# Kernel optimization log

Measured on AMD Instinct MI355X. Metric: run time of the kernel, lower is better.

## Reference

```python
import jax, jax.numpy as jnp
import numpy as np

NEG = -1.0e30  # stand-in for -inf, safe under logaddexp in fp32
DEN_SCALE = 1.0


def _ctc_forward(logp, targets, in_lens, tgt_lens):
    """Log-semiring forward (tot score) over the numerator lattice:
    CTC topology composed with the linear target FSA. logp: [B,T,C] (blank=0),
    targets: [B,U] in [1, C-1]. Returns [B] numerator log-scores."""
    B, T, C = logp.shape
    U = targets.shape[1]
    S = 2 * U + 1  # extended label sequence: blank-interleaved
    ext = jnp.zeros((B, S), dtype=jnp.int32).at[:, 1::2].set(targets.astype(jnp.int32))
    # skip transition s-2 -> s allowed only for non-blank, non-repeated labels
    skip_ok = jnp.concatenate(
        [jnp.zeros((B, 2), dtype=bool), (ext[:, 2:] != 0) & (ext[:, 2:] != ext[:, :-2])],
        axis=1,
    )
    emit0 = jnp.take_along_axis(logp[:, 0], ext, axis=1)  # [B,S]
    alpha = jnp.full((B, S), NEG, dtype=logp.dtype)
    alpha = alpha.at[:, 0].set(emit0[:, 0]).at[:, 1].set(emit0[:, 1])
    logp_t = jnp.swapaxes(logp, 0, 1)  # [T,B,C]

    def step(alpha, xs):
        t, lp = xs
        a1 = jnp.concatenate([jnp.full((B, 1), NEG, alpha.dtype), alpha[:, :-1]], axis=1)
        a2 = jnp.concatenate([jnp.full((B, 2), NEG, alpha.dtype), alpha[:, :-2]], axis=1)
        cand = jnp.logaddexp(jnp.logaddexp(alpha, a1), jnp.where(skip_ok, a2, NEG))
        new = cand + jnp.take_along_axis(lp, ext, axis=1)
        alpha = jnp.where((t < in_lens)[:, None], new, alpha)  # freeze past utterance end
        return alpha, None

    alpha, _ = jax.lax.scan(step, alpha, (jnp.arange(1, T), logp_t[1:]))
    last = (2 * tgt_lens).astype(jnp.int32)  # final states: last blank / last label
    a_last = jnp.take_along_axis(alpha, last[:, None], axis=1)[:, 0]
    a_prev = jnp.take_along_axis(alpha, (last - 1)[:, None], axis=1)[:, 0]
    return jnp.logaddexp(a_last, a_prev)


def _den_forward(logp, trans, start, in_lens):
    """Log-semiring forward over the dense denominator graph (bigram token LM):
    states = token classes, transition log-weights trans[C,C]. Returns [B]."""
    B, T, C = logp.shape
    alpha = start[None, :] + logp[:, 0]  # [B,C]
    logp_t = jnp.swapaxes(logp, 0, 1)  # [T,B,C]

    def step(alpha, xs):
        t, lp = xs
        new = jax.nn.logsumexp(alpha[:, :, None] + trans[None], axis=1) + lp
        alpha = jnp.where((t < in_lens)[:, None], new, alpha)
        return alpha, None

    alpha, _ = jax.lax.scan(step, alpha, (jnp.arange(1, T), logp_t[1:]))
    return jax.nn.logsumexp(alpha, axis=1)


def setup_inputs() -> dict:
    key = jax.random.key(0)
    ks = jax.random.split(key, 6)
    B, T, C, U = 32, 2000, 256, 200
    log_probs = jax.nn.log_softmax(jax.random.normal(ks[0], (B, T, C), dtype=jnp.float32), axis=-1)
    targets = jax.random.randint(ks[1], (B, U), 1, C)
    input_lengths = jax.random.randint(ks[2], (B,), T // 2, T + 1)
    target_lengths = jax.random.randint(ks[3], (B,), U // 2, U + 1)
    den_transitions = jax.random.normal(ks[4], (C, C), dtype=jnp.float32) * 0.1
    den_start = jax.random.normal(ks[5], (C,), dtype=jnp.float32) * 0.1
    return {
        "log_probs": log_probs,
        "targets": targets,
        "input_lengths": input_lengths,
        "target_lengths": target_lengths,
        "den_transitions": den_transitions,
        "den_start": den_start,
    }


def reference(log_probs, targets, input_lengths, target_lengths, den_transitions, den_start):
    logp = jax.nn.log_softmax(log_probs, axis=-1)  # idempotent if already normalized
    B, T, C = logp.shape
    U = targets.shape[1]
    in_lens = jnp.clip(input_lengths, 2 * U + 1, T).astype(jnp.int32)
    tgt_lens = jnp.clip(target_lengths, 1, U).astype(jnp.int32)
    tgt = jnp.clip(targets, 1, C - 1)  # blank=0 excluded from targets
    num = _ctc_forward(logp, tgt, in_lens, tgt_lens)
    den = _den_forward(logp, den_transitions, den_start, in_lens)
    tot = num - DEN_SCALE * den  # LF-MMI per-utterance objective
    valid = tot > 0.5 * NEG  # mimic get_tot_objf_and_num_frames -inf filtering
    n = jnp.maximum(jnp.sum(valid), 1)
    return -jnp.sum(jnp.where(valid, tot, 0.0)) / n
```

## Files before the change

kernel.cpp:

```cpp
#include <hip/hip_runtime.h>
#include <stdint.h>
#include <stddef.h>

#define NEGF (-1.0e30f)

typedef __attribute__((ext_vector_type(2))) _Float16 half2_t;
typedef uint32_t u32x16 __attribute__((ext_vector_type(16)));

constexpr int Bn = 32;
constexpr int Tn = 2000;
constexpr int Cn = 256;
constexpr int Un = 200;
constexpr int Sn = 2 * Un + 1;
constexpr float Kn = 4096.0f;

__device__ __forceinline__ float fdot2f(uint32_t a, uint32_t b, float c) {
  half2_t ha = __builtin_bit_cast(half2_t, a);
  half2_t hb = __builtin_bit_cast(half2_t, b);
#if __has_builtin(__builtin_amdgcn_fdot2)
  return __builtin_amdgcn_fdot2(ha, hb, c, false);
#else
  return c + (float)ha.x * (float)hb.x + (float)ha.y * (float)hb.y;
#endif
}

template <int CTRL>
__device__ __forceinline__ float dppf(float x) {
#if __has_builtin(__builtin_amdgcn_update_dpp)
  int xi = __builtin_bit_cast(int, x);
  int y = __builtin_amdgcn_update_dpp(0, xi, CTRL, 0xF, 0xF, false);
  return __builtin_bit_cast(float, y);
#else
  return x;
#endif
}
#define dpp_x1(v) dppf<0xB1>(v)
#define dpp_x2(v) dppf<0x4E>(v)
#define dpp_x7(v) dppf<0x141>(v)

__device__ __forceinline__ uint32_t packe(float a, float b) {
  half2_t h;
  h.x = (_Float16)a;
  h.y = (_Float16)b;
  return __builtin_bit_cast(uint32_t, h);
}

__device__ __forceinline__ float lse3(float a, float b, float c) {
  float m = fmaxf(fmaxf(a, b), c);
  return m + __logf(__expf(a - m) + __expf(b - m) + __expf(c - m));
}

__device__ __forceinline__ int clampi(int v, int lo, int hi) {
  return v < lo ? lo : (v > hi ? hi : v);
}

__device__ __forceinline__ void barrier_nodrain() {
  asm volatile("s_waitcnt lgkmcnt(0)" ::: "memory");
  __builtin_amdgcn_s_barrier();
  asm volatile("" ::: "memory");
}

__global__ __launch_bounds__(256)
__attribute__((amdgpu_waves_per_eu(1, 1)))
void fwd_kernel(
    const float* __restrict__ logp, const int* __restrict__ targets,
    const int* __restrict__ in_lens, const int* __restrict__ tgt_lens,
    const float* __restrict__ trans, const float* __restrict__ start,
    float* __restrict__ ws) {
  const int tid = threadIdx.x;
  const int bid = blockIdx.x;

  if (bid < Bn) {
    const int b = bid;
    const int L = clampi(in_lens[b], Sn, Tn);
    const int q = tid & 7;
    const int u = tid >> 3;
    const int jw = u + 32 * q;

    __shared__ __align__(16) char eaLDS[2 * 8 * 80];
    __shared__ float sred[4];

    const float* trow = trans;
#define EP(c, m) packe(__expf(trow[(32 * q + 2 * (m)) * Cn + (c)]), \
                       __expf(trow[(32 * q + 2 * (m) + 1) * Cn + (c)]))
#define MKCOL(c)                                                          \
  (u32x16){EP(c, 0),  EP(c, 1),  EP(c, 2),  EP(c, 3),  EP(c, 4),          \
           EP(c, 5),  EP(c, 6),  EP(c, 7),  EP(c, 8),  EP(c, 9),          \
           EP(c, 10), EP(c, 11), EP(c, 12), EP(c, 13), EP(c, 14), EP(c, 15)}
    u32x16 E0 = MKCOL(u + 0);
    u32x16 E1 = MKCOL(u + 32);
    u32x16 E2 = MKCOL(u + 64);
    u32x16 E3 = MKCOL(u + 96);
    u32x16 E4 = MKCOL(u + 128);
    u32x16 E5 = MKCOL(u + 160);
    u32x16 E6 = MKCOL(u + 192);
    u32x16 E7 = MKCOL(u + 224);
#undef MKCOL
#undef EP

    const float* lpb = logp + (size_t)b * Tn * Cn;
    const char* rbase0 = eaLDS + 80 * q;
    char* wptr0 = eaLDS + 80 * q + 2 * u;

    float G = -__logf(Kn);
    *(_Float16*)(wptr0) = (_Float16)(Kn * __expf(start[jw] + lpb[jw]));
    float lp0 = lpb[Cn + jw];
    float lp1 = lpb[(size_t)2 * Cn + jw];
    __syncthreads();

    const uint32_t ONE2 = 0x3C003C00u;
    const bool q4 = (q & 4) != 0, q2 = (q & 2) != 0, q1 = (q & 1) != 0;

    for (int t = 1; t < L; ++t) {
      const int pr = (t - 1) & 1, pw = t & 1;
      const float lp_cur = lp0;
      lp0 = lp1;
      const int tpre = (t + 2 < L) ? t + 2 : L - 1;
      lp1 = lpb[(size_t)tpre * Cn + jw];
      const float p = __expf(lp_cur);

      const uint4* eap = (const uint4*)(rbase0 + pr * 640);
      float a0 = 0.f, a1 = 0.f, a2 = 0.f, a3 = 0.f;
      float a4 = 0.f, a5 = 0.f, a6 = 0.f, a7 = 0.f;
      half2_t zpk = {(_Float16)0.f, (_Float16)0.f};
#define B2(x) __builtin_bit_cast(half2_t, x)
#define DOT8(idx, ev)               \
  a0 = fdot2f(E0[idx], ev, a0);     \
  a1 = fdot2f(E1[idx], ev, a1);     \
  a2 = fdot2f(E2[idx], ev, a2);     \
  a3 = fdot2f(E3[idx], ev, a3);     \
  a4 = fdot2f(E4[idx], ev, a4);     \
  a5 = fdot2f(E5[idx], ev, a5);     \
  a6 = fdot2f(E6[idx], ev, a6);     \
  a7 = fdot2f(E7[idx], ev, a7);
#define DOTQ(m4)                                                      \
  {                                                                   \
    const uint4 e4 = eap[m4];                                         \
    DOT8(4 * (m4) + 0, e4.x)                                          \
    DOT8(4 * (m4) + 1, e4.y)                                          \
    DOT8(4 * (m4) + 2, e4.z)                                          \
    DOT8(4 * (m4) + 3, e4.w)                                          \
    zpk = zpk + ((B2(e4.x) + B2(e4.y)) + (B2(e4.z) + B2(e4.w)));      \
  }
      DOTQ(0)
      DOTQ(1)
      DOTQ(2)
      DOTQ(3)
#undef DOTQ
#undef DOT8

      float zc = fdot2f(ONE2, __builtin_bit_cast(uint32_t, zpk), 0.f);
      zc += dpp_x1(zc);
      zc += dpp_x2(zc);
      zc += dpp_x7(zc);

      float g, t0, t1, t2, t3, w0, w1, s;
      g = q4 ? a0 : a4;  t0 = (q4 ? a4 : a0) + dpp_x7(g);
      g = q4 ? a1 : a5;  t1 = (q4 ? a5 : a1) + dpp_x7(g);
      g = q4 ? a2 : a6;  t2 = (q4 ? a6 : a2) + dpp_x7(g);
      g = q4 ? a3 : a7;  t3 = (q4 ? a7 : a3) + dpp_x7(g);
      g = q2 ? t0 : t2;  w0 = (q2 ? t2 : t0) + dpp_x2(g);
      g = q2 ? t1 : t3;  w1 = (q2 ? t3 : t1) + dpp_x2(g);
      g = q1 ? w0 : w1;  s  = (q1 ? w1 : w0) + dpp_x1(g);

      const float invZ = Kn * __frcp_rn(zc);
      G -= __logf(invZ);
      *(_Float16*)(wptr0 + pw * 640) = (_Float16)(s * p * invZ);
      barrier_nodrain();
    }

    {
      const int pL = (L - 1) & 1;
      const char* fb = eaLDS + pL * 640;
      float e = (float)(*(const _Float16*)(fb + 80 * (tid >> 5) + 2 * (tid & 31)));
#pragma unroll
      for (int off = 32; off >= 1; off >>= 1) e += __shfl_xor(e, off, 64);
      const int lane = tid & 63, wid = tid >> 6;
      if (lane == 0) sred[wid] = e;
      __syncthreads();
      if (tid == 0) {
        float ssum = (sred[0] + sred[1]) + (sred[2] + sred[3]);
        ws[Bn + b] = G + __logf(ssum);
      }
    }
  } else {
    const int b = bid - Bn;
    const int L = clampi(in_lens[b], Sn, Tn);
    const int tl = clampi(tgt_lens[b], 1, Un);

    __shared__ float abuf[2][Sn + 3];
    const float* lpb = logp + (size_t)b * Tn * Cn;
    const int* tgtb = targets + b * Un;

    const int s1 = tid;
    const int s2 = tid + 256;
    int e1 = 0, e2 = 0;
    bool k1 = false, k2 = false;
    if (s1 & 1) {
      const int uu = (s1 - 1) >> 1;
      e1 = clampi(tgtb[uu], 1, Cn - 1);
      if (uu > 0) k1 = (e1 != clampi(tgtb[uu - 1], 1, Cn - 1));
    }
    if ((s2 < Sn) && (s2 & 1)) {
      const int uu = (s2 - 1) >> 1;
      e2 = clampi(tgtb[uu], 1, Cn - 1);
      k2 = (e2 != clampi(tgtb[uu - 1], 1, Cn - 1));
    }

    abuf[0][s1 + 2] = (s1 == 0) ? lpb[0] : (s1 == 1 ? lpb[e1] : NEGF);
    if (s2 < Sn) abuf[0][s2 + 2] = NEGF;
    if (tid < 2) { abuf[0][tid] = NEGF; abuf[1][tid] = NEGF; }
    float pe1_0 = lpb[Cn + e1];
    float pe2_0 = lpb[Cn + e2];
    float pe1_1 = lpb[(size_t)2 * Cn + e1];
    float pe2_1 = lpb[(size_t)2 * Cn + e2];
    __syncthreads();

    int cur = 0;
    for (int t = 1; t < L; ++t) {
      const float em1 = pe1_0, em2 = pe2_0;
      pe1_0 = pe1_1;
      pe2_0 = pe2_1;
      const int tpre = (t + 2 < L) ? t + 2 : L - 1;
      pe1_1 = lpb[(size_t)tpre * Cn + e1];
      pe2_1 = lpb[(size_t)tpre * Cn + e2];
      const float* A = abuf[cur];
      float* Bv = abuf[cur ^ 1];
      {
        const float x = A[s1 + 2], y = A[s1 + 1];
        const float z = k1 ? A[s1] : NEGF;
        Bv[s1 + 2] = lse3(x, y, z) + em1;
      }
      if (s2 < Sn) {
        const float x = A[s2 + 2], y = A[s2 + 1];
        const float z = k2 ? A[s2] : NEGF;
        Bv[s2 + 2] = lse3(x, y, z) + em2;
      }
      barrier_nodrain();
      cur ^= 1;
    }
    if (tid == 0) {
      const int l = 2 * tl;
      const float x = abuf[cur][l + 2], y = abuf[cur][l + 1];
      const float m = fmaxf(x, y);
      ws[b] = m + __logf(__expf(x - m) + __expf(y - m));
    }
  }
}

__global__ void finalize_kernel(const float* __restrict__ ws,
                                float* __restrict__ out) {
  const int tid = threadIdx.x;
  float tot = 0.f, cnt = 0.f;
  if (tid < Bn) {
    const float tv = ws[tid] - ws[Bn + tid];
    const bool valid = tv > 0.5f * NEGF;
    tot = valid ? tv : 0.f;
    cnt = valid ? 1.f : 0.f;
  }
#pragma unroll
  for (int off = 32; off >= 1; off >>= 1) {
    tot += __shfl_xor(tot, off, 64);
    cnt += __shfl_xor(cnt, off, 64);
  }
  if (tid == 0) out[0] = -tot / fmaxf(cnt, 1.f);
}

extern "C" void kernel_launch(void* const* d_in, const int* in_sizes, int n_in,
                              void* d_out, int out_size, void* d_ws, size_t ws_size,
                              hipStream_t stream) {
  const float* logp = (const float*)d_in[0];
  const int* targets = (const int*)d_in[1];
  const int* in_lens = (const int*)d_in[2];
  const int* tgt_lens = (const int*)d_in[3];
  const float* trans = (const float*)d_in[4];
  const float* start = (const float*)d_in[5];
  float* ws = (float*)d_ws;
  float* out = (float*)d_out;
  (void)in_sizes; (void)n_in; (void)out_size; (void)ws_size;

  fwd_kernel<<<dim3(2 * Bn), dim3(256), 0, stream>>>(
      logp, targets, in_lens, tgt_lens, trans, start, ws);
  finalize_kernel<<<dim3(1), dim3(64), 0, stream>>>(ws, out);
}
```

Baseline: 1.046 ms.

## Double threads per block to halve per-thread work in both forward recursions

Raises the block size from 256 to 512 threads. In the denominator path each thread now holds 4 transition columns instead of 8 and does half the fdot2 work per step, with a shorter DPP reduction tree. In the CTC path each thread now handles one lattice state instead of two. The serial per-timestep latency should drop, but the per-step barrier now has to synchronize 8 waves instead of 4, and waves_per_eu is raised to 2.

```diff
diff --git a/kernel.cpp b/kernel.cpp
--- a/kernel.cpp
+++ b/kernel.cpp
@@ -60,8 +60,8 @@
   asm volatile("" ::: "memory");
 }
 
-__global__ __launch_bounds__(256)
-__attribute__((amdgpu_waves_per_eu(1, 1)))
+__global__ __launch_bounds__(512)
+__attribute__((amdgpu_waves_per_eu(2, 2)))
 void fwd_kernel(
     const float* __restrict__ logp, const int* __restrict__ targets,
     const int* __restrict__ in_lens, const int* __restrict__ tgt_lens,
@@ -75,10 +75,13 @@
     const int L = clampi(in_lens[b], Sn, Tn);
     const int q = tid & 7;
     const int u = tid >> 3;
-    const int jw = u + 32 * q;
+    const bool q4 = (q & 4) != 0, q2 = (q & 2) != 0, q1 = (q & 1) != 0;
+    (void)q1;
+    const int kk = (q4 ? 2 : 0) + (q2 ? 1 : 0);
+    const int jw = u + 64 * kk;
 
     __shared__ __align__(16) char eaLDS[2 * 8 * 80];
-    __shared__ float sred[4];
+    __shared__ float sred[8];
 
     const float* trow = trans;
 #define EP(c, m) packe(__expf(trow[(32 * q + 2 * (m)) * Cn + (c)]), \
@@ -88,19 +91,15 @@
            EP(c, 5),  EP(c, 6),  EP(c, 7),  EP(c, 8),  EP(c, 9),          \
            EP(c, 10), EP(c, 11), EP(c, 12), EP(c, 13), EP(c, 14), EP(c, 15)}
     u32x16 E0 = MKCOL(u + 0);
-    u32x16 E1 = MKCOL(u + 32);
-    u32x16 E2 = MKCOL(u + 64);
-    u32x16 E3 = MKCOL(u + 96);
-    u32x16 E4 = MKCOL(u + 128);
-    u32x16 E5 = MKCOL(u + 160);
-    u32x16 E6 = MKCOL(u + 192);
-    u32x16 E7 = MKCOL(u + 224);
+    u32x16 E1 = MKCOL(u + 64);
+    u32x16 E2 = MKCOL(u + 128);
+    u32x16 E3 = MKCOL(u + 192);
 #undef MKCOL
 #undef EP
 
     const float* lpb = logp + (size_t)b * Tn * Cn;
     const char* rbase0 = eaLDS + 80 * q;
-    char* wptr0 = eaLDS + 80 * q + 2 * u;
+    char* wptr0 = eaLDS + 80 * (2 * kk + (u >> 5)) + 2 * (u & 31);
 
     float G = -__logf(Kn);
     *(_Float16*)(wptr0) = (_Float16)(Kn * __expf(start[jw] + lpb[jw]));
@@ -109,7 +108,6 @@
     __syncthreads();
 
     const uint32_t ONE2 = 0x3C003C00u;
-    const bool q4 = (q & 4) != 0, q2 = (q & 2) != 0, q1 = (q & 1) != 0;
 
     for (int t = 1; t < L; ++t) {
       const int pr = (t - 1) & 1, pw = t & 1;
@@ -121,25 +119,20 @@
 
       const uint4* eap = (const uint4*)(rbase0 + pr * 640);
       float a0 = 0.f, a1 = 0.f, a2 = 0.f, a3 = 0.f;
-      float a4 = 0.f, a5 = 0.f, a6 = 0.f, a7 = 0.f;
       half2_t zpk = {(_Float16)0.f, (_Float16)0.f};
 #define B2(x) __builtin_bit_cast(half2_t, x)
-#define DOT8(idx, ev)               \
+#define DOT4(idx, ev)               \
   a0 = fdot2f(E0[idx], ev, a0);     \
   a1 = fdot2f(E1[idx], ev, a1);     \
   a2 = fdot2f(E2[idx], ev, a2);     \
-  a3 = fdot2f(E3[idx], ev, a3);     \
-  a4 = fdot2f(E4[idx], ev, a4);     \
-  a5 = fdot2f(E5[idx], ev, a5);     \
-  a6 = fdot2f(E6[idx], ev, a6);     \
-  a7 = fdot2f(E7[idx], ev, a7);
+  a3 = fdot2f(E3[idx], ev, a3);
 #define DOTQ(m4)                                                      \
   {                                                                   \
     const uint4 e4 = eap[m4];                                         \
-    DOT8(4 * (m4) + 0, e4.x)                                          \
-    DOT8(4 * (m4) + 1, e4.y)                                          \
-    DOT8(4 * (m4) + 2, e4.z)                                          \
-    DOT8(4 * (m4) + 3, e4.w)                                          \
+    DOT4(4 * (m4) + 0, e4.x)                                          \
+    DOT4(4 * (m4) + 1, e4.y)                                          \
+    DOT4(4 * (m4) + 2, e4.z)                                          \
+    DOT4(4 * (m4) + 3, e4.w)                                          \
     zpk = zpk + ((B2(e4.x) + B2(e4.y)) + (B2(e4.z) + B2(e4.w)));      \
   }
       DOTQ(0)
@@ -147,21 +140,18 @@
       DOTQ(2)
       DOTQ(3)
 #undef DOTQ
-#undef DOT8
+#undef DOT4
 
       float zc = fdot2f(ONE2, __builtin_bit_cast(uint32_t, zpk), 0.f);
       zc += dpp_x1(zc);
       zc += dpp_x2(zc);
       zc += dpp_x7(zc);
 
-      float g, t0, t1, t2, t3, w0, w1, s;
-      g = q4 ? a0 : a4;  t0 = (q4 ? a4 : a0) + dpp_x7(g);
-      g = q4 ? a1 : a5;  t1 = (q4 ? a5 : a1) + dpp_x7(g);
-      g = q4 ? a2 : a6;  t2 = (q4 ? a6 : a2) + dpp_x7(g);
-      g = q4 ? a3 : a7;  t3 = (q4 ? a7 : a3) + dpp_x7(g);
-      g = q2 ? t0 : t2;  w0 = (q2 ? t2 : t0) + dpp_x2(g);
-      g = q2 ? t1 : t3;  w1 = (q2 ? t3 : t1) + dpp_x2(g);
-      g = q1 ? w0 : w1;  s  = (q1 ? w1 : w0) + dpp_x1(g);
+      float g, t0, t1, w, s;
+      g = q4 ? a0 : a2;  t0 = (q4 ? a2 : a0) + dpp_x7(g);
+      g = q4 ? a1 : a3;  t1 = (q4 ? a3 : a1) + dpp_x7(g);
+      g = q2 ? t0 : t1;  w  = (q2 ? t1 : t0) + dpp_x2(g);
+      s = w + dpp_x1(w);
 
       const float invZ = Kn * __frcp_rn(zc);
       G -= __logf(invZ);
@@ -172,14 +162,17 @@
     {
       const int pL = (L - 1) & 1;
       const char* fb = eaLDS + pL * 640;
-      float e = (float)(*(const _Float16*)(fb + 80 * (tid >> 5) + 2 * (tid & 31)));
+      float e = 0.f;
+      if (tid < 256)
+        e = (float)(*(const _Float16*)(fb + 80 * (tid >> 5) + 2 * (tid & 31)));
 #pragma unroll
       for (int off = 32; off >= 1; off >>= 1) e += __shfl_xor(e, off, 64);
       const int lane = tid & 63, wid = tid >> 6;
       if (lane == 0) sred[wid] = e;
       __syncthreads();
       if (tid == 0) {
-        float ssum = (sred[0] + sred[1]) + (sred[2] + sred[3]);
+        float ssum = ((sred[0] + sred[1]) + (sred[2] + sred[3])) +
+                     ((sred[4] + sred[5]) + (sred[6] + sred[7]));
         ws[Bn + b] = G + __logf(ssum);
       }
     }
@@ -193,48 +186,33 @@
     const int* tgtb = targets + b * Un;
 
     const int s1 = tid;
-    const int s2 = tid + 256;
-    int e1 = 0, e2 = 0;
-    bool k1 = false, k2 = false;
-    if (s1 & 1) {
+    int e1 = 0;
+    bool k1 = false;
+    const bool act = (s1 < Sn);
+    if (act && (s1 & 1)) {
       const int uu = (s1 - 1) >> 1;
       e1 = clampi(tgtb[uu], 1, Cn - 1);
       if (uu > 0) k1 = (e1 != clampi(tgtb[uu - 1], 1, Cn - 1));
     }
-    if ((s2 < Sn) && (s2 & 1)) {
-      const int uu = (s2 - 1) >> 1;
-      e2 = clampi(tgtb[uu], 1, Cn - 1);
-      k2 = (e2 != clampi(tgtb[uu - 1], 1, Cn - 1));
-    }
-
-    abuf[0][s1 + 2] = (s1 == 0) ? lpb[0] : (s1 == 1 ? lpb[e1] : NEGF);
-    if (s2 < Sn) abuf[0][s2 + 2] = NEGF;
+
+    if (act) abuf[0][s1 + 2] = (s1 == 0) ? lpb[0] : (s1 == 1 ? lpb[e1] : NEGF);
     if (tid < 2) { abuf[0][tid] = NEGF; abuf[1][tid] = NEGF; }
-    float pe1_0 = lpb[Cn + e1];
-    float pe2_0 = lpb[Cn + e2];
-    float pe1_1 = lpb[(size_t)2 * Cn + e1];
-    float pe2_1 = lpb[(size_t)2 * Cn + e2];
+    float pe0 = lpb[Cn + e1];
+    float pe1 = lpb[(size_t)2 * Cn + e1];
     __syncthreads();
 
     int cur = 0;
     for (int t = 1; t < L; ++t) {
-      const float em1 = pe1_0, em2 = pe2_0;
-      pe1_0 = pe1_1;
-      pe2_0 = pe2_1;
+      const float em1 = pe0;
+      pe0 = pe1;
       const int tpre = (t + 2 < L) ? t + 2 : L - 1;
-      pe1_1 = lpb[(size_t)tpre * Cn + e1];
-      pe2_1 = lpb[(size_t)tpre * Cn + e2];
+      pe1 = lpb[(size_t)tpre * Cn + e1];
       const float* A = abuf[cur];
       float* Bv = abuf[cur ^ 1];
-      {
+      if (act) {
         const float x = A[s1 + 2], y = A[s1 + 1];
         const float z = k1 ? A[s1] : NEGF;
         Bv[s1 + 2] = lse3(x, y, z) + em1;
-      }
-      if (s2 < Sn) {
-        const float x = A[s2 + 2], y = A[s2 + 1];
-        const float z = k2 ? A[s2] : NEGF;
-        Bv[s2 + 2] = lse3(x, y, z) + em2;
       }
       barrier_nodrain();
       cur ^= 1;
@@ -279,7 +257,7 @@
   float* out = (float*)d_out;
   (void)in_sizes; (void)n_in; (void)out_size; (void)ws_size;
 
-  fwd_kernel<<<dim3(2 * Bn), dim3(256), 0, stream>>>(
+  fwd_kernel<<<dim3(2 * Bn), dim3(512), 0, stream>>>(
       logp, targets, in_lens, tgt_lens, trans, start, ws);
   finalize_kernel<<<dim3(1), dim3(64), 0, stream>>>(ws, out);
 }
```

Result: slower. 1.218 ms (+16.4%).

## Batch denominator forward 16 utterances per block using MFMA f16 matmuls

Applied to the files above, without the earlier changes.

Each denominator step is now a matrix product: a block handles 16 utterances at once and computes alpha times exp(trans) with MFMA 16x16x32 f16 instructions. This replaces the per-utterance fdot2 and DPP reduction across 32 blocks. The goal is to cut per-step latency and block count by using the matrix cores, so only 2 blocks handle the denominator. In exchange, every utterance in a block runs for the block's longest input length with masking, LDS is swizzled to avoid bank conflicts, and each step now has two barriers.

```diff
diff --git a/kernel.cpp b/kernel.cpp
--- a/kernel.cpp
+++ b/kernel.cpp
@@ -5,7 +5,9 @@
 #define NEGF (-1.0e30f)
 
 typedef __attribute__((ext_vector_type(2))) _Float16 half2_t;
-typedef uint32_t u32x16 __attribute__((ext_vector_type(16)));
+typedef __attribute__((ext_vector_type(8))) _Float16 f16x8;
+typedef __attribute__((ext_vector_type(4))) float f32x4;
+typedef __attribute__((ext_vector_type(4))) uint32_t u32x4;
 
 constexpr int Bn = 32;
 constexpr int Tn = 2000;
@@ -13,6 +15,8 @@
 constexpr int Un = 200;
 constexpr int Sn = 2 * Un + 1;
 constexpr float Kn = 4096.0f;
+constexpr int NBD = 2;
+constexpr int BPB = 16;
 
 __device__ __forceinline__ float fdot2f(uint32_t a, uint32_t b, float c) {
   half2_t ha = __builtin_bit_cast(half2_t, a);
@@ -24,20 +28,6 @@
 #endif
 }
 
-template <int CTRL>
-__device__ __forceinline__ float dppf(float x) {
-#if __has_builtin(__builtin_amdgcn_update_dpp)
-  int xi = __builtin_bit_cast(int, x);
-  int y = __builtin_amdgcn_update_dpp(0, xi, CTRL, 0xF, 0xF, false);
-  return __builtin_bit_cast(float, y);
-#else
-  return x;
-#endif
-}
-#define dpp_x1(v) dppf<0xB1>(v)
-#define dpp_x2(v) dppf<0x4E>(v)
-#define dpp_x7(v) dppf<0x141>(v)
-
 __device__ __forceinline__ uint32_t packe(float a, float b) {
   half2_t h;
   h.x = (_Float16)a;
@@ -54,11 +44,21 @@
   return v < lo ? lo : (v > hi ? hi : v);
 }
 
+__device__ __forceinline__ f32x4 exp4(f32x4 v) {
+  f32x4 r;
+  r[0] = __expf(v[0]);
+  r[1] = __expf(v[1]);
+  r[2] = __expf(v[2]);
+  r[3] = __expf(v[3]);
+  return r;
+}
+
 __device__ __forceinline__ void barrier_nodrain() {
   asm volatile("s_waitcnt lgkmcnt(0)" ::: "memory");
   __builtin_amdgcn_s_barrier();
   asm volatile("" ::: "memory");
 }
+
 
 __global__ __launch_bounds__(256)
 __attribute__((amdgpu_waves_per_eu(1, 1)))
@@ -70,121 +70,158 @@
   const int tid = threadIdx.x;
   const int bid = blockIdx.x;
 
-  if (bid < Bn) {
-    const int b = bid;
-    const int L = clampi(in_lens[b], Sn, Tn);
-    const int q = tid & 7;
-    const int u = tid >> 3;
-    const int jw = u + 32 * q;
-
-    __shared__ __align__(16) char eaLDS[2 * 8 * 80];
-    __shared__ float sred[4];
-
-    const float* trow = trans;
-#define EP(c, m) packe(__expf(trow[(32 * q + 2 * (m)) * Cn + (c)]), \
-                       __expf(trow[(32 * q + 2 * (m) + 1) * Cn + (c)]))
-#define MKCOL(c)                                                          \
-  (u32x16){EP(c, 0),  EP(c, 1),  EP(c, 2),  EP(c, 3),  EP(c, 4),          \
-           EP(c, 5),  EP(c, 6),  EP(c, 7),  EP(c, 8),  EP(c, 9),          \
-           EP(c, 10), EP(c, 11), EP(c, 12), EP(c, 13), EP(c, 14), EP(c, 15)}
-    u32x16 E0 = MKCOL(u + 0);
-    u32x16 E1 = MKCOL(u + 32);
-    u32x16 E2 = MKCOL(u + 64);
-    u32x16 E3 = MKCOL(u + 96);
-    u32x16 E4 = MKCOL(u + 128);
-    u32x16 E5 = MKCOL(u + 160);
-    u32x16 E6 = MKCOL(u + 192);
-    u32x16 E7 = MKCOL(u + 224);
-#undef MKCOL
-#undef EP
-
-    const float* lpb = logp + (size_t)b * Tn * Cn;
-    const char* rbase0 = eaLDS + 80 * q;
-    char* wptr0 = eaLDS + 80 * q + 2 * u;
-
+  if (bid < NBD) {
+    __shared__ __align__(16) char Abuf[16 * 512];
+    __shared__ float stage[32 * 258];
+
+    const int lane = tid & 63;
+    const int w = tid >> 6;
+    const int br = lane & 15;
+    const int g = lane >> 4;
+    const int gb = bid * BPB + br;
+    const int jbase = 64 * w;
+
+    const int Lv = clampi(in_lens[gb], Sn, Tn);
+    int Lblk = Lv;
+#pragma unroll
+    for (int off = 1; off < 16; off <<= 1) {
+      const int o = __shfl_xor(Lblk, off, 64);
+      Lblk = Lblk > o ? Lblk : o;
+    }
+
+    f16x8 E[4][8];
+#pragma unroll
+    for (int kt = 0; kt < 8; ++kt) {
+      const float* src = trans + (size_t)(32 * kt) * Cn;
+#pragma unroll
+      for (int jj = 0; jj < 8; ++jj) {
+        const int i4 = tid + jj * 256;
+        const float4 v = *(const float4*)(src + 4 * (size_t)i4);
+        const int r = i4 >> 6, c = (i4 & 63) * 4;
+        float* dst = stage + r * 258 + c;
+        *(float2*)(dst) = make_float2(v.x, v.y);
+        *(float2*)(dst + 2) = make_float2(v.z, v.w);
+      }
+      __syncthreads();
+#pragma unroll
+      for (int mt = 0; mt < 4; ++mt) {
+        const int j = jbase + 16 * mt + br;
+        f16x8 e;
+#pragma unroll
+        for (int jj = 0; jj < 8; ++jj)
+          e[jj] = (_Float16)__expf(stage[(8 * g + jj) * 258 + j]);
+        E[mt][kt] = e;
+      }
+      __syncthreads();
+    }
+
+    const char* rdp[8];
+#pragma unroll
+    for (int kt = 0; kt < 8; ++kt)
+      rdp[kt] = Abuf + br * 512 + ((64 * kt + 16 * g) ^ ((br & 7) << 4));
+    char* wrp[4];
+#pragma unroll
+    for (int mt = 0; mt < 4; ++mt)
+      wrp[mt] = Abuf + br * 512 + ((2 * (jbase + 16 * mt + 4 * g)) ^ ((br & 7) << 4));
+
+    {
+      const int b0 = tid & 15;
+      const int c0 = (tid >> 4) * 16;
+      const float* lpr = logp + (size_t)(bid * BPB + b0) * Tn * Cn;
+#pragma unroll
+      for (int jj = 0; jj < 16; jj += 2) {
+        const int j = c0 + jj;
+        const float v0 = Kn * __expf(start[j] + lpr[j]);
+        const float v1 = Kn * __expf(start[j + 1] + lpr[j + 1]);
+        *(uint32_t*)(Abuf + b0 * 512 + ((2 * j) ^ ((b0 & 7) << 4))) = packe(v0, v1);
+      }
+    }
+
+    const float* lpl = logp + (size_t)gb * Tn * Cn + (jbase + 4 * g);
+    f32x4 P0[4], P1[4];
+#pragma unroll
+    for (int mt = 0; mt < 4; ++mt) {
+      P0[mt] = exp4(*(const f32x4*)(lpl + (size_t)1 * Cn + 16 * mt));
+      P1[mt] = *(const f32x4*)(lpl + (size_t)2 * Cn + 16 * mt);
+    }
     float G = -__logf(Kn);
-    *(_Float16*)(wptr0) = (_Float16)(Kn * __expf(start[jw] + lpb[jw]));
-    float lp0 = lpb[Cn + jw];
-    float lp1 = lpb[(size_t)2 * Cn + jw];
     __syncthreads();
 
     const uint32_t ONE2 = 0x3C003C00u;
-    const bool q4 = (q & 4) != 0, q2 = (q & 2) != 0, q1 = (q & 1) != 0;
-
-    for (int t = 1; t < L; ++t) {
-      const int pr = (t - 1) & 1, pw = t & 1;
-      const float lp_cur = lp0;
-      lp0 = lp1;
-      const int tpre = (t + 2 < L) ? t + 2 : L - 1;
-      lp1 = lpb[(size_t)tpre * Cn + jw];
-      const float p = __expf(lp_cur);
-
-      const uint4* eap = (const uint4*)(rbase0 + pr * 640);
-      float a0 = 0.f, a1 = 0.f, a2 = 0.f, a3 = 0.f;
-      float a4 = 0.f, a5 = 0.f, a6 = 0.f, a7 = 0.f;
-      half2_t zpk = {(_Float16)0.f, (_Float16)0.f};
-#define B2(x) __builtin_bit_cast(half2_t, x)
-#define DOT8(idx, ev)               \
-  a0 = fdot2f(E0[idx], ev, a0);     \
-  a1 = fdot2f(E1[idx], ev, a1);     \
-  a2 = fdot2f(E2[idx], ev, a2);     \
-  a3 = fdot2f(E3[idx], ev, a3);     \
-  a4 = fdot2f(E4[idx], ev, a4);     \
-  a5 = fdot2f(E5[idx], ev, a5);     \
-  a6 = fdot2f(E6[idx], ev, a6);     \
-  a7 = fdot2f(E7[idx], ev, a7);
-#define DOTQ(m4)                                                      \
-  {                                                                   \
-    const uint4 e4 = eap[m4];                                         \
-    DOT8(4 * (m4) + 0, e4.x)                                          \
-    DOT8(4 * (m4) + 1, e4.y)                                          \
-    DOT8(4 * (m4) + 2, e4.z)                                          \
-    DOT8(4 * (m4) + 3, e4.w)                                          \
-    zpk = zpk + ((B2(e4.x) + B2(e4.y)) + (B2(e4.z) + B2(e4.w)));      \
-  }
-      DOTQ(0)
-      DOTQ(1)
-      DOTQ(2)
-      DOTQ(3)
-#undef DOTQ
-#undef DOT8
-
-      float zc = fdot2f(ONE2, __builtin_bit_cast(uint32_t, zpk), 0.f);
-      zc += dpp_x1(zc);
-      zc += dpp_x2(zc);
-      zc += dpp_x7(zc);
-
-      float g, t0, t1, t2, t3, w0, w1, s;
-      g = q4 ? a0 : a4;  t0 = (q4 ? a4 : a0) + dpp_x7(g);
-      g = q4 ? a1 : a5;  t1 = (q4 ? a5 : a1) + dpp_x7(g);
-      g = q4 ? a2 : a6;  t2 = (q4 ? a6 : a2) + dpp_x7(g);
-      g = q4 ? a3 : a7;  t3 = (q4 ? a7 : a3) + dpp_x7(g);
-      g = q2 ? t0 : t2;  w0 = (q2 ? t2 : t0) + dpp_x2(g);
-      g = q2 ? t1 : t3;  w1 = (q2 ? t3 : t1) + dpp_x2(g);
-      g = q1 ? w0 : w1;  s  = (q1 ? w1 : w0) + dpp_x1(g);
-
+
+    for (int t = 1; t < Lblk; ++t) {
+      f16x8 Bf[8];
+#pragma unroll
+      for (int kt = 0; kt < 8; ++kt) Bf[kt] = *(const f16x8*)rdp[kt];
+
+      half2_t zp = {(_Float16)0.f, (_Float16)0.f};
+#pragma unroll
+      for (int kt = 0; kt < 8; ++kt) {
+        const u32x4 q = __builtin_bit_cast(u32x4, Bf[kt]);
+        zp = zp + ((__builtin_bit_cast(half2_t, q.x) + __builtin_bit_cast(half2_t, q.y)) +
+                   (__builtin_bit_cast(half2_t, q.z) + __builtin_bit_cast(half2_t, q.w)));
+      }
+      float zc = fdot2f(ONE2, __builtin_bit_cast(uint32_t, zp), 0.f);
+      zc += __shfl_xor(zc, 16, 64);
+      zc += __shfl_xor(zc, 32, 64);
       const float invZ = Kn * __frcp_rn(zc);
-      G -= __logf(invZ);
-      *(_Float16*)(wptr0 + pw * 640) = (_Float16)(s * p * invZ);
+
+      f32x4 acc[4];
+#pragma unroll
+      for (int mt = 0; mt < 4; ++mt) {
+        f32x4 a = {0.f, 0.f, 0.f, 0.f};
+#pragma unroll
+        for (int kt = 0; kt < 8; ++kt)
+          a = __builtin_amdgcn_mfma_f32_16x16x32_f16(E[mt][kt], Bf[kt], a, 0, 0, 0);
+        acc[mt] = a;
+      }
+
+      if (t < Lv) G -= __logf(invZ);
+
       barrier_nodrain();
+
+      if (t < Lv) {
+#pragma unroll
+        for (int mt = 0; mt < 4; ++mt) {
+          const float s0 = acc[mt][0] * P0[mt][0] * invZ;
+          const float s1 = acc[mt][1] * P0[mt][1] * invZ;
+          const float s2 = acc[mt][2] * P0[mt][2] * invZ;
+          const float s3 = acc[mt][3] * P0[mt][3] * invZ;
+          uint2 pk;
+          pk.x = packe(s0, s1);
+          pk.y = packe(s2, s3);
+          *(uint2*)wrp[mt] = pk;
+        }
+      }
+
+      const int tpre = (t + 2 < Lblk) ? t + 2 : Lblk - 1;
+      const float* pp = lpl + (size_t)tpre * Cn;
+#pragma unroll
+      for (int mt = 0; mt < 4; ++mt) {
+        P0[mt] = exp4(P1[mt]);
+        P1[mt] = *(const f32x4*)(pp + 16 * mt);
+      }
+      barrier_nodrain();
     }
 
     {
-      const int pL = (L - 1) & 1;
-      const char* fb = eaLDS + pL * 640;
-      float e = (float)(*(const _Float16*)(fb + 80 * (tid >> 5) + 2 * (tid & 31)));
-#pragma unroll
-      for (int off = 32; off >= 1; off >>= 1) e += __shfl_xor(e, off, 64);
-      const int lane = tid & 63, wid = tid >> 6;
-      if (lane == 0) sred[wid] = e;
-      __syncthreads();
-      if (tid == 0) {
-        float ssum = (sred[0] + sred[1]) + (sred[2] + sred[3]);
-        ws[Bn + b] = G + __logf(ssum);
-      }
+      f16x8 Bf[8];
+#pragma unroll
+      for (int kt = 0; kt < 8; ++kt) Bf[kt] = *(const f16x8*)rdp[kt];
+      half2_t zp = {(_Float16)0.f, (_Float16)0.f};
+#pragma unroll
+      for (int kt = 0; kt < 8; ++kt) {
+        const u32x4 q = __builtin_bit_cast(u32x4, Bf[kt]);
+        zp = zp + ((__builtin_bit_cast(half2_t, q.x) + __builtin_bit_cast(half2_t, q.y)) +
+                   (__builtin_bit_cast(half2_t, q.z) + __builtin_bit_cast(half2_t, q.w)));
+      }
+      float rs = fdot2f(ONE2, __builtin_bit_cast(uint32_t, zp), 0.f);
+      rs += __shfl_xor(rs, 16, 64);
+      rs += __shfl_xor(rs, 32, 64);
+      if (tid < 16) ws[Bn + bid * BPB + tid] = G + __logf(rs);
     }
   } else {
-    const int b = bid - Bn;
+    const int b = bid - NBD;
     const int L = clampi(in_lens[b], Sn, Tn);
     const int tl = clampi(tgt_lens[b], 1, Un);
 
@@ -279,7 +316,7 @@
   float* out = (float*)d_out;
   (void)in_sizes; (void)n_in; (void)out_size; (void)ws_size;
 
-  fwd_kernel<<<dim3(2 * Bn), dim3(256), 0, stream>>>(
+  fwd_kernel<<<dim3(NBD + Bn), dim3(256), 0, stream>>>(
       logp, targets, in_lens, tgt_lens, trans, start, ws);
   finalize_kernel<<<dim3(1), dim3(64), 0, stream>>>(ws, out);
 }
```

Result: slower. 1.576 ms (+50.7%).

## Merge numerator and denominator forward passes into one 512-thread block per utterance

Applied to the files above, without the earlier changes.

Instead of launching separate blocks for the CTC numerator and the dense denominator recursion, each utterance now gets one 512-thread block. The first 256 threads run the denominator recursion and the second 256 run the numerator recursion, sharing one barrier per time step. The aim is to halve the block count and co-locate both recursions on one CU. In exchange, every step's barrier now spans eight waves and both recursions advance in lockstep. The two workloads also compete for one CU's issue slots and registers under the new waves-per-EU setting.

```diff
diff --git a/kernel.cpp b/kernel.cpp
--- a/kernel.cpp
+++ b/kernel.cpp
@@ -60,25 +60,41 @@
   asm volatile("" ::: "memory");
 }
 
-__global__ __launch_bounds__(256)
-__attribute__((amdgpu_waves_per_eu(1, 1)))
+
+__global__ __launch_bounds__(512)
+__attribute__((amdgpu_waves_per_eu(2, 2)))
 void fwd_kernel(
     const float* __restrict__ logp, const int* __restrict__ targets,
     const int* __restrict__ in_lens, const int* __restrict__ tgt_lens,
     const float* __restrict__ trans, const float* __restrict__ start,
     float* __restrict__ ws) {
   const int tid = threadIdx.x;
-  const int bid = blockIdx.x;
-
-  if (bid < Bn) {
-    const int b = bid;
-    const int L = clampi(in_lens[b], Sn, Tn);
+  const int b = blockIdx.x;
+  const int L = clampi(in_lens[b], Sn, Tn);
+  const bool isden = tid < 256;
+
+  __shared__ __align__(16) char eaLDS[2 * 8 * 80];
+  __shared__ float sred[4];
+  __shared__ float abuf[2][Sn + 3];
+
+  const float* lpb = logp + (size_t)b * Tn * Cn;
+
+  u32x16 E0, E1, E2, E3, E4, E5, E6, E7;
+  float G = 0.f, lp0 = 0.f, lp1 = 0.f;
+  const char* rbase0 = nullptr;
+  char* wptr0 = nullptr;
+  int dq = 0;
+  int e1 = 0, e2 = 0;
+  bool k1 = false, k2 = false;
+  float pe1_0 = 0.f, pe2_0 = 0.f, pe1_1 = 0.f, pe2_1 = 0.f;
+  int s2v = 0;
+  int cur = 0;
+
+  if (isden) {
     const int q = tid & 7;
     const int u = tid >> 3;
     const int jw = u + 32 * q;
-
-    __shared__ __align__(16) char eaLDS[2 * 8 * 80];
-    __shared__ float sred[4];
+    dq = q;
 
     const float* trow = trans;
 #define EP(c, m) packe(__expf(trow[(32 * q + 2 * (m)) * Cn + (c)]), \
@@ -87,32 +103,57 @@
   (u32x16){EP(c, 0),  EP(c, 1),  EP(c, 2),  EP(c, 3),  EP(c, 4),          \
            EP(c, 5),  EP(c, 6),  EP(c, 7),  EP(c, 8),  EP(c, 9),          \
            EP(c, 10), EP(c, 11), EP(c, 12), EP(c, 13), EP(c, 14), EP(c, 15)}
-    u32x16 E0 = MKCOL(u + 0);
-    u32x16 E1 = MKCOL(u + 32);
-    u32x16 E2 = MKCOL(u + 64);
-    u32x16 E3 = MKCOL(u + 96);
-    u32x16 E4 = MKCOL(u + 128);
-    u32x16 E5 = MKCOL(u + 160);
-    u32x16 E6 = MKCOL(u + 192);
-    u32x16 E7 = MKCOL(u + 224);
+    E0 = MKCOL(u + 0);
+    E1 = MKCOL(u + 32);
+    E2 = MKCOL(u + 64);
+    E3 = MKCOL(u + 96);
+    E4 = MKCOL(u + 128);
+    E5 = MKCOL(u + 160);
+    E6 = MKCOL(u + 192);
+    E7 = MKCOL(u + 224);
 #undef MKCOL
 #undef EP
 
-    const float* lpb = logp + (size_t)b * Tn * Cn;
-    const char* rbase0 = eaLDS + 80 * q;
-    char* wptr0 = eaLDS + 80 * q + 2 * u;
-
-    float G = -__logf(Kn);
+    rbase0 = eaLDS + 80 * q;
+    wptr0 = eaLDS + 80 * q + 2 * u;
+
+    G = -__logf(Kn);
     *(_Float16*)(wptr0) = (_Float16)(Kn * __expf(start[jw] + lpb[jw]));
-    float lp0 = lpb[Cn + jw];
-    float lp1 = lpb[(size_t)2 * Cn + jw];
-    __syncthreads();
-
-    const uint32_t ONE2 = 0x3C003C00u;
-    const bool q4 = (q & 4) != 0, q2 = (q & 2) != 0, q1 = (q & 1) != 0;
-
-    for (int t = 1; t < L; ++t) {
+    lp0 = lpb[Cn + jw];
+    lp1 = lpb[(size_t)2 * Cn + jw];
+  } else {
+    const int nt = tid - 256;
+    const int* tgtb = targets + b * Un;
+    const int s1 = nt;
+    s2v = nt + 256;
+    if (s1 & 1) {
+      const int uu = (s1 - 1) >> 1;
+      e1 = clampi(tgtb[uu], 1, Cn - 1);
+      if (uu > 0) k1 = (e1 != clampi(tgtb[uu - 1], 1, Cn - 1));
+    }
+    if ((s2v < Sn) && (s2v & 1)) {
+      const int uu = (s2v - 1) >> 1;
+      e2 = clampi(tgtb[uu], 1, Cn - 1);
+      k2 = (e2 != clampi(tgtb[uu - 1], 1, Cn - 1));
+    }
+
+    abuf[0][s1 + 2] = (s1 == 0) ? lpb[0] : (s1 == 1 ? lpb[e1] : NEGF);
+    if (s2v < Sn) abuf[0][s2v + 2] = NEGF;
+    if (nt < 2) { abuf[0][nt] = NEGF; abuf[1][nt] = NEGF; }
+    pe1_0 = lpb[Cn + e1];
+    pe2_0 = lpb[Cn + e2];
+    pe1_1 = lpb[(size_t)2 * Cn + e1];
+    pe2_1 = lpb[(size_t)2 * Cn + e2];
+  }
+  __syncthreads();
+
+  const uint32_t ONE2 = 0x3C003C00u;
+  const bool q4 = (dq & 4) != 0, q2 = (dq & 2) != 0, q1 = (dq & 1) != 0;
+
+  for (int t = 1; t < L; ++t) {
+    if (isden) {
       const int pr = (t - 1) & 1, pw = t & 1;
+      const int jw = (tid >> 3) + 32 * dq;
       const float lp_cur = lp0;
       lp0 = lp1;
       const int tpre = (t + 2 < L) ? t + 2 : L - 1;
@@ -148,6 +189,7 @@
       DOTQ(3)
 #undef DOTQ
 #undef DOT8
+#undef B2
 
       float zc = fdot2f(ONE2, __builtin_bit_cast(uint32_t, zpk), 0.f);
       zc += dpp_x1(zc);
@@ -166,58 +208,9 @@
       const float invZ = Kn * __frcp_rn(zc);
       G -= __logf(invZ);
       *(_Float16*)(wptr0 + pw * 640) = (_Float16)(s * p * invZ);
-      barrier_nodrain();
-    }
-
-    {
-      const int pL = (L - 1) & 1;
-      const char* fb = eaLDS + pL * 640;
-      float e = (float)(*(const _Float16*)(fb + 80 * (tid >> 5) + 2 * (tid & 31)));
-#pragma unroll
-      for (int off = 32; off >= 1; off >>= 1) e += __shfl_xor(e, off, 64);
-      const int lane = tid & 63, wid = tid >> 6;
-      if (lane == 0) sred[wid] = e;
-      __syncthreads();
-      if (tid == 0) {
-        float ssum = (sred[0] + sred[1]) + (sred[2] + sred[3]);
-        ws[Bn + b] = G + __logf(ssum);
-      }
-    }
-  } else {
-    const int b = bid - Bn;
-    const int L = clampi(in_lens[b], Sn, Tn);
-    const int tl = clampi(tgt_lens[b], 1, Un);
-
-    __shared__ float abuf[2][Sn + 3];
-    const float* lpb = logp + (size_t)b * Tn * Cn;
-    const int* tgtb = targets + b * Un;
-
-    const int s1 = tid;
-    const int s2 = tid + 256;
-    int e1 = 0, e2 = 0;
-    bool k1 = false, k2 = false;
-    if (s1 & 1) {
-      const int uu = (s1 - 1) >> 1;
-      e1 = clampi(tgtb[uu], 1, Cn - 1);
-      if (uu > 0) k1 = (e1 != clampi(tgtb[uu - 1], 1, Cn - 1));
-    }
-    if ((s2 < Sn) && (s2 & 1)) {
-      const int uu = (s2 - 1) >> 1;
-      e2 = clampi(tgtb[uu], 1, Cn - 1);
-      k2 = (e2 != clampi(tgtb[uu - 1], 1, Cn - 1));
-    }
-
-    abuf[0][s1 + 2] = (s1 == 0) ? lpb[0] : (s1 == 1 ? lpb[e1] : NEGF);
-    if (s2 < Sn) abuf[0][s2 + 2] = NEGF;
-    if (tid < 2) { abuf[0][tid] = NEGF; abuf[1][tid] = NEGF; }
-    float pe1_0 = lpb[Cn + e1];
-    float pe2_0 = lpb[Cn + e2];
-    float pe1_1 = lpb[(size_t)2 * Cn + e1];
-    float pe2_1 = lpb[(size_t)2 * Cn + e2];
-    __syncthreads();
-
-    int cur = 0;
-    for (int t = 1; t < L; ++t) {
+    } else {
+      const int nt = tid - 256;
+      const int s1 = nt;
       const float em1 = pe1_0, em2 = pe2_0;
       pe1_0 = pe1_1;
       pe2_0 = pe2_1;
@@ -231,20 +224,36 @@
         const float z = k1 ? A[s1] : NEGF;
         Bv[s1 + 2] = lse3(x, y, z) + em1;
       }
-      if (s2 < Sn) {
-        const float x = A[s2 + 2], y = A[s2 + 1];
-        const float z = k2 ? A[s2] : NEGF;
-        Bv[s2 + 2] = lse3(x, y, z) + em2;
+      if (s2v < Sn) {
+        const float x = A[s2v + 2], y = A[s2v + 1];
+        const float z = k2 ? A[s2v] : NEGF;
+        Bv[s2v + 2] = lse3(x, y, z) + em2;
       }
-      barrier_nodrain();
       cur ^= 1;
     }
-    if (tid == 0) {
-      const int l = 2 * tl;
-      const float x = abuf[cur][l + 2], y = abuf[cur][l + 1];
-      const float m = fmaxf(x, y);
-      ws[b] = m + __logf(__expf(x - m) + __expf(y - m));
-    }
+    barrier_nodrain();
+  }
+
+  if (isden) {
+    const int pL = (L - 1) & 1;
+    const char* fb = eaLDS + pL * 640;
+    float e = (float)(*(const _Float16*)(fb + 80 * (tid >> 5) + 2 * (tid & 31)));
+#pragma unroll
+    for (int off = 32; off >= 1; off >>= 1) e += __shfl_xor(e, off, 64);
+    const int lane = tid & 63, wid = tid >> 6;
+    if (lane == 0) sred[wid] = e;
+  }
+  __syncthreads();
+  if (tid == 0) {
+    float ssum = (sred[0] + sred[1]) + (sred[2] + sred[3]);
+    ws[Bn + b] = G + __logf(ssum);
+  }
+  if (tid == 256) {
+    const int tl = clampi(tgt_lens[b], 1, Un);
+    const int l = 2 * tl;
+    const float x = abuf[cur][l + 2], y = abuf[cur][l + 1];
+    const float m = fmaxf(x, y);
+    ws[b] = m + __logf(__expf(x - m) + __expf(y - m));
   }
 }
 
@@ -279,7 +288,7 @@
   float* out = (float*)d_out;
   (void)in_sizes; (void)n_in; (void)out_size; (void)ws_size;
 
-  fwd_kernel<<<dim3(2 * Bn), dim3(256), 0, stream>>>(
+  fwd_kernel<<<dim3(Bn), dim3(512), 0, stream>>>(
       logp, targets, in_lens, tgt_lens, trans, start, ws);
   finalize_kernel<<<dim3(1), dim3(64), 0, stream>>>(ws, out);
 }
```

Result: slower. 1.396 ms (+33.5%).
